# Kernel tuning notes

Measured on AMD Instinct MI355X. Metric: run time of the kernel, lower is better.

The kernel has to match this reference:

```python
import jax, jax.numpy as jnp
import numpy as np

SMOOTH = 1e-6
K = 64  # num_selection_features


def setup_inputs() -> dict:
    key = jax.random.key(0)
    kx, kw, kb = jax.random.split(key, 3)
    x = jax.random.normal(kx, (8, 256, 128, 128), dtype=jnp.float32)
    # 1x1 conv: Conv2d(K, 1) -> weight [1, K, 1, 1]; store as [K] and scalar bias
    w = jax.random.normal(kw, (K,), dtype=jnp.float32) * (1.0 / np.sqrt(K))
    b = jax.random.normal(kb, (1,), dtype=jnp.float32) * 0.01
    return {"x": x, "w": w, "b": b}


def reference(x, w, b):
    B, C, H, W = x.shape
    s = jax.nn.sigmoid(x)
    uncertainty = -s * jnp.log(s + SMOOTH)           # [B,C,H,W]
    score = jnp.mean(uncertainty, axis=(2, 3))       # [B,C]
    # topk smallest -> top_k of negated score
    _, idx = jax.lax.top_k(-score, K)                # [B,K]
    selected = jnp.take_along_axis(x, idx[:, :, None, None], axis=1)  # [B,K,H,W]
    # 1x1 conv (K->1) + sigmoid
    attn = jax.nn.sigmoid(jnp.einsum('bkhw,k->bhw', selected, w) + b[0])  # [B,H,W]
    return x * attn[:, None, :, :]
```

## Files before the change

kernel.cpp:

```cpp
#include <hip/hip_runtime.h>

constexpr int B  = 8;
constexpr int C  = 256;
constexpr int HW = 128 * 128;
constexpr int K  = 64;
#define SMOOTH 1e-6f

__device__ __forceinline__ float uncert(float v) {
    float s = 1.0f / (1.0f + expf(-v));
    return -s * logf(s + SMOOTH);
}

__global__ void score_kernel(const float* __restrict__ x, float* __restrict__ score) {
    const int plane = blockIdx.x;
    const float4* xp = (const float4*)(x + (size_t)plane * HW);
    const int t = threadIdx.x;

    float acc = 0.0f;
#pragma unroll
    for (int i = 0; i < 16; ++i) {
        float4 v = xp[t + i * 256];
        acc += uncert(v.x) + uncert(v.y) + uncert(v.z) + uncert(v.w);
    }
#pragma unroll
    for (int off = 32; off > 0; off >>= 1) acc += __shfl_down(acc, off, 64);

    __shared__ float smem[4];
    if ((t & 63) == 0) smem[t >> 6] = acc;
    __syncthreads();
    if (t == 0) score[plane] = (smem[0] + smem[1] + smem[2] + smem[3]) * (1.0f / HW);
}

__global__ void topk_kernel(const float* __restrict__ score, int* __restrict__ sel) {
    const int b = blockIdx.x;
    const int t = threadIdx.x;
    __shared__ float sc[C];
    sc[t] = score[b * C + t];
    __syncthreads();

    const float my = sc[t];
    int rank = 0;
#pragma unroll 8
    for (int j = 0; j < C; ++j) {
        float o = sc[j];
        rank += (o < my) || (o == my && j < t);
    }
    if (rank < K) sel[b * K + rank] = t;
}

__global__ void attn_kernel(const float* __restrict__ x, const int* __restrict__ sel,
                            const float* __restrict__ w, const float* __restrict__ bias,
                            float* __restrict__ attn) {
    const int b     = blockIdx.x >> 4;
    const int chunk = blockIdx.x & 15;
    const int t     = threadIdx.x;

    __shared__ float ws[K];
    __shared__ int   chs[K];
    if (t < K) { ws[t] = w[t]; chs[t] = sel[b * K + t]; }
    __syncthreads();

    const int p4 = chunk * 256 + t;
    const float4* xb = (const float4*)(x + (size_t)b * C * HW);

    float ax = 0.f, ay = 0.f, az = 0.f, aw = 0.f;
#pragma unroll 8
    for (int k = 0; k < K; ++k) {
        float4 v = xb[(size_t)chs[k] * (HW / 4) + p4];
        float wk = ws[k];
        ax += wk * v.x; ay += wk * v.y; az += wk * v.z; aw += wk * v.w;
    }
    const float b0 = bias[0];
    float4 o;
    o.x = 1.0f / (1.0f + expf(-(ax + b0)));
    o.y = 1.0f / (1.0f + expf(-(ay + b0)));
    o.z = 1.0f / (1.0f + expf(-(az + b0)));
    o.w = 1.0f / (1.0f + expf(-(aw + b0)));
    ((float4*)attn)[((size_t)b << 12) + p4] = o;
}

__global__ void mul_kernel(const float* __restrict__ x, const float* __restrict__ attn,
                           float* __restrict__ out) {
    const size_t i = (size_t)blockIdx.x * blockDim.x + threadIdx.x;
    const float4* x4 = (const float4*)x;
    const float4* a4 = (const float4*)attn;
    float4 v = x4[i];
    float4 a = a4[((i >> 20) << 12) | (i & 4095)];
    float4 o; o.x = v.x * a.x; o.y = v.y * a.y; o.z = v.z * a.z; o.w = v.w * a.w;
    ((float4*)out)[i] = o;
}

extern "C" void kernel_launch(void* const* d_in, const int* in_sizes, int n_in,
                              void* d_out, int out_size, void* d_ws, size_t ws_size,
                              hipStream_t stream) {
    const float* x    = (const float*)d_in[0];
    const float* w    = (const float*)d_in[1];
    const float* bias = (const float*)d_in[2];
    float* out = (float*)d_out;

    char* ws = (char*)d_ws;
    float* score = (float*)ws;
    int*   sel   = (int*)(ws + 8192);
    float* attn  = (float*)(ws + 16384);

    score_kernel<<<B * C, 256, 0, stream>>>(x, score);
    topk_kernel<<<B, C, 0, stream>>>(score, sel);
    attn_kernel<<<B * 16, 256, 0, stream>>>(x, sel, w, bias, attn);
    const int n4 = B * C * HW / 4;
    mul_kernel<<<n4 / 256, 256, 0, stream>>>(x, attn, out);
}
```

Measured before the change: 269.9 us.

## Fuse top-k, attention conv and broadcast multiply into one kernel; use fast math

Merges the top-k selection, the 1x1 conv with sigmoid, and the final elementwise multiply into a single kernel. Each block recomputes the rank-based top-k for its batch, splits the 64 selected channels across four waves for the weighted sum, reduces the partials through LDS, and then multiplies a 64-float4 pixel chunk across all 256 channels using nontemporal stores. The score kernel switches to __expf/__logf and hardware rcp. This removes two launches and the attn round-trip through memory, at the cost of redundant top-k work in every block, a small 512-block grid that may underfill the GPU, and slightly lower math precision.

```diff
diff --git a/kernel.cpp b/kernel.cpp
--- a/kernel.cpp
+++ b/kernel.cpp
@@ -4,14 +4,17 @@
 constexpr int C  = 256;
 constexpr int HW = 128 * 128;
 constexpr int K  = 64;
-#define SMOOTH 1e-6f
 
-__device__ __forceinline__ float uncert(float v) {
-    float s = 1.0f / (1.0f + expf(-v));
-    return -s * logf(s + SMOOTH);
+typedef float vf4 __attribute__((ext_vector_type(4)));
+
+__device__ __forceinline__ float uncert_fast(float x) {
+    float t = __expf(-x);
+    float s = __builtin_amdgcn_rcpf(1.0f + t);
+    return -s * __logf(s + 1e-6f);
 }
 
-__global__ void score_kernel(const float* __restrict__ x, float* __restrict__ score) {
+__global__ __launch_bounds__(256) void score_kernel(const float* __restrict__ x,
+                                                    float* __restrict__ score) {
     const int plane = blockIdx.x;
     const float4* xp = (const float4*)(x + (size_t)plane * HW);
     const int t = threadIdx.x;
@@ -20,74 +23,86 @@
 #pragma unroll
     for (int i = 0; i < 16; ++i) {
         float4 v = xp[t + i * 256];
-        acc += uncert(v.x) + uncert(v.y) + uncert(v.z) + uncert(v.w);
+        acc += uncert_fast(v.x) + uncert_fast(v.y) + uncert_fast(v.z) + uncert_fast(v.w);
     }
 #pragma unroll
     for (int off = 32; off > 0; off >>= 1) acc += __shfl_down(acc, off, 64);
 
-    __shared__ float smem[4];
-    if ((t & 63) == 0) smem[t >> 6] = acc;
+    __shared__ float sm[4];
+    if ((t & 63) == 0) sm[t >> 6] = acc;
     __syncthreads();
-    if (t == 0) score[plane] = (smem[0] + smem[1] + smem[2] + smem[3]) * (1.0f / HW);
+    if (t == 0) score[plane] = (sm[0] + sm[1] + sm[2] + sm[3]) * (1.0f / HW);
 }
 
-__global__ void topk_kernel(const float* __restrict__ score, int* __restrict__ sel) {
-    const int b = blockIdx.x;
-    const int t = threadIdx.x;
+__global__ __launch_bounds__(256) void fused_kernel(
+    const float* __restrict__ x, const float* __restrict__ score,
+    const float* __restrict__ w, const float* __restrict__ bias,
+    float* __restrict__ out)
+{
+    const int b     = blockIdx.x >> 6;
+    const int chunk = blockIdx.x & 63;
+    const int t  = threadIdx.x;
+    const int wv = t >> 6, ln = t & 63;
+
     __shared__ float sc[C];
+    __shared__ float wsh[K];
+    __shared__ int   chs[K];
+    __shared__ vf4   part[4][64];
+    __shared__ vf4   attn_s[64];
+
     sc[t] = score[b * C + t];
+    if (t < K) wsh[t] = w[t];
     __syncthreads();
 
-    const float my = sc[t];
-    int rank = 0;
-#pragma unroll 8
-    for (int j = 0; j < C; ++j) {
-        float o = sc[j];
-        rank += (o < my) || (o == my && j < t);
+    {
+        const float my = sc[t];
+        int rank = 0;
+#pragma unroll 16
+        for (int j = 0; j < C; ++j) {
+            float o = sc[j];
+            rank += (o < my) || (o == my && j < t);
+        }
+        if (rank < K) chs[rank] = t;
     }
-    if (rank < K) sel[b * K + rank] = t;
-}
-
-__global__ void attn_kernel(const float* __restrict__ x, const int* __restrict__ sel,
-                            const float* __restrict__ w, const float* __restrict__ bias,
-                            float* __restrict__ attn) {
-    const int b     = blockIdx.x >> 4;
-    const int chunk = blockIdx.x & 15;
-    const int t     = threadIdx.x;
-
-    __shared__ float ws[K];
-    __shared__ int   chs[K];
-    if (t < K) { ws[t] = w[t]; chs[t] = sel[b * K + t]; }
     __syncthreads();
 
-    const int p4 = chunk * 256 + t;
-    const float4* xb = (const float4*)(x + (size_t)b * C * HW);
+    const float* xb = x + (size_t)b * C * HW;
+    const int p4 = (chunk << 6) + ln;
 
-    float ax = 0.f, ay = 0.f, az = 0.f, aw = 0.f;
-#pragma unroll 8
-    for (int k = 0; k < K; ++k) {
-        float4 v = xb[(size_t)chs[k] * (HW / 4) + p4];
-        float wk = ws[k];
-        ax += wk * v.x; ay += wk * v.y; az += wk * v.z; aw += wk * v.w;
+    vf4 acc = (vf4)0.0f;
+#pragma unroll
+    for (int kk = 0; kk < 16; ++kk) {
+        const int k = (wv << 4) + kk;
+        const float wk = wsh[k];
+        vf4 v = ((const vf4*)(xb + (size_t)chs[k] * HW))[p4];
+        acc += wk * v;
     }
-    const float b0 = bias[0];
-    float4 o;
-    o.x = 1.0f / (1.0f + expf(-(ax + b0)));
-    o.y = 1.0f / (1.0f + expf(-(ay + b0)));
-    o.z = 1.0f / (1.0f + expf(-(az + b0)));
-    o.w = 1.0f / (1.0f + expf(-(aw + b0)));
-    ((float4*)attn)[((size_t)b << 12) + p4] = o;
-}
+    part[wv][ln] = acc;
+    __syncthreads();
 
-__global__ void mul_kernel(const float* __restrict__ x, const float* __restrict__ attn,
-                           float* __restrict__ out) {
-    const size_t i = (size_t)blockIdx.x * blockDim.x + threadIdx.x;
-    const float4* x4 = (const float4*)x;
-    const float4* a4 = (const float4*)attn;
-    float4 v = x4[i];
-    float4 a = a4[((i >> 20) << 12) | (i & 4095)];
-    float4 o; o.x = v.x * a.x; o.y = v.y * a.y; o.z = v.z * a.z; o.w = v.w * a.w;
-    ((float4*)out)[i] = o;
+    if (wv == 0) {
+        vf4 a = part[0][ln] + part[1][ln] + part[2][ln] + part[3][ln];
+        const float b0 = bias[0];
+        vf4 o;
+        o.x = __builtin_amdgcn_rcpf(1.0f + __expf(-(a.x + b0)));
+        o.y = __builtin_amdgcn_rcpf(1.0f + __expf(-(a.y + b0)));
+        o.z = __builtin_amdgcn_rcpf(1.0f + __expf(-(a.z + b0)));
+        o.w = __builtin_amdgcn_rcpf(1.0f + __expf(-(a.w + b0)));
+        attn_s[ln] = o;
+    }
+    __syncthreads();
+    const vf4 am = attn_s[ln];
+
+    const vf4* xb4 = (const vf4*)xb;
+    vf4* ob4 = (vf4*)(out + (size_t)b * C * HW);
+#pragma unroll 4
+    for (int j = 0; j < 64; ++j) {
+        const int c = (wv << 6) + j;
+        const size_t idx = (size_t)c * (HW / 4) + p4;
+        vf4 v = xb4[idx];
+        vf4 o = v * am;
+        __builtin_nontemporal_store(o, ob4 + idx);
+    }
 }
 
 extern "C" void kernel_launch(void* const* d_in, const int* in_sizes, int n_in,
@@ -98,14 +113,8 @@
     const float* bias = (const float*)d_in[2];
     float* out = (float*)d_out;
 
-    char* ws = (char*)d_ws;
-    float* score = (float*)ws;
-    int*   sel   = (int*)(ws + 8192);
-    float* attn  = (float*)(ws + 16384);
+    float* score = (float*)d_ws;
 
     score_kernel<<<B * C, 256, 0, stream>>>(x, score);
-    topk_kernel<<<B, C, 0, stream>>>(score, sel);
-    attn_kernel<<<B * 16, 256, 0, stream>>>(x, sel, w, bias, attn);
-    const int n4 = B * C * HW / 4;
-    mul_kernel<<<n4 / 256, 256, 0, stream>>>(x, attn, out);
+    fused_kernel<<<B * 64, 256, 0, stream>>>(x, score, w, bias, out);
 }
```

New measurement: 279.1 us. 1.03x slower.
